# Kernel optimization log

Measured on AMD Instinct MI355X. Metric: run time of the kernel, lower is better.

The kernel has to match this reference:

```python
import jax, jax.numpy as jnp
import numpy as np

KER = 8

def _gelu(x):
    return jax.nn.gelu(x, approximate=False)

def _conv3x3(x, w, b):
    y = jax.lax.conv_general_dilated(x, w, (1, 1), 'SAME',
                                     dimension_numbers=('NCHW', 'OIHW', 'NCHW'))
    return y + b[None, :, None, None]

def _unfold(x):
    # F.unfold(kernel=8, stride=8): [B,C,H,W] -> [B, C*64, L], C-major then kh,kw
    B, C, H, W = x.shape
    Hb, Wb = H // KER, W // KER
    p = x.reshape(B, C, Hb, KER, Wb, KER).transpose(0, 1, 3, 5, 2, 4)
    return p.reshape(B, C * KER * KER, Hb * Wb)

def _fold(cols, H, W):
    # inverse of _unfold (non-overlapping patches)
    B, CK, L = cols.shape
    C = CK // (KER * KER)
    Hb, Wb = H // KER, W // KER
    p = cols.reshape(B, C, KER, KER, Hb, Wb).transpose(0, 1, 4, 2, 5, 3)
    return p.reshape(B, C, H, W)

def _bn(x, g, b, eps=1e-5):
    # train-mode BatchNorm1d on [B, C, L]: stats over (B, L) per channel
    m = x.mean(axis=(0, 2), keepdims=True)
    v = x.var(axis=(0, 2), keepdims=True)
    return (x - m) * jax.lax.rsqrt(v + eps) * g[None, :, None] + b[None, :, None]


def setup_inputs() -> dict:
    key = jax.random.key(0)
    ks = jax.random.split(key, 10)
    ind, d, hid = 64, 1024, 256
    f = lambda k, s: jax.random.normal(k, s, dtype=jnp.float32) * 0.02
    return {
        'feat': jax.random.normal(ks[0], (4, ind, 256, 256), dtype=jnp.float32),
        'w_enc': f(ks[1], (ind, ind, 3, 3)), 'b_enc': jnp.zeros((ind,), jnp.float32),
        'w_k': f(ks[2], (ind, ind, 3, 3)), 'b_k': jnp.zeros((ind,), jnp.float32),
        'w_v': f(ks[3], (ind, ind, 3, 3)), 'b_v': jnp.zeros((ind,), jnp.float32),
        'fcq_w': f(ks[4], (d, ind * KER * KER)), 'fcq_b': jnp.zeros((d,), jnp.float32),
        'fck_w': f(ks[5], (d, ind * KER * KER)), 'fck_b': jnp.zeros((d,), jnp.float32),
        'bnq_g': jnp.ones((d,), jnp.float32), 'bnq_b': jnp.zeros((d,), jnp.float32),
        'bnk_g': jnp.ones((d,), jnp.float32), 'bnk_b': jnp.zeros((d,), jnp.float32),
        'ff1_w': f(ks[6], (hid, ind)), 'ff1_b': jnp.zeros((hid,), jnp.float32),
        'ff2_w': f(ks[7], (ind, hid)), 'ff2_b': jnp.zeros((ind,), jnp.float32),
    }


def reference(feat, w_enc, b_enc, w_k, b_k, w_v, b_v,
              fcq_w, fcq_b, fck_w, fck_b, bnq_g, bnq_b, bnk_g, bnk_b,
              ff1_w, ff1_b, ff2_w, ff2_b):
    B, C, H, W = feat.shape
    fk = _gelu(_conv3x3(feat, w_k, b_k))
    fv = _gelu(_conv3x3(feat, w_v, b_v))
    refer = _gelu(_conv3x3(feat, w_enc, b_enc))
    q_un = _unfold(refer).transpose(0, 2, 1)   # [B, L, C*64]
    k_un = _unfold(fk).transpose(0, 2, 1)
    v_un = _unfold(fv).transpose(0, 2, 1)
    q = jnp.einsum('blc,dc->bld', q_un, fcq_w) + fcq_b
    q = _bn(q.transpose(0, 2, 1), bnq_g, bnq_b).transpose(0, 2, 1)  # [B, L, 1024]
    k = jnp.einsum('blc,dc->bld', k_un, fck_w) + fck_b
    k = _bn(k.transpose(0, 2, 1), bnk_g, bnk_b).transpose(0, 2, 1)
    scores = jnp.einsum('bld,bmd->blm', q, k) / jnp.sqrt(jnp.float32(q.shape[2]))
    attn = jax.nn.softmax(scores, axis=2)
    out = jnp.einsum('blm,bmc->blc', attn, v_un).transpose(0, 2, 1)  # [B, C*64, L]
    out = _fold(out, H, W)
    h = _gelu(jnp.einsum('bchw,oc->bohw', out, ff1_w) + ff1_b[None, :, None, None])
    h = _gelu(jnp.einsum('bchw,oc->bohw', h, ff2_w) + ff2_b[None, :, None, None])
    return h + feat
```

## Files before the change

kernel.cpp:

```cpp
#include <hip/hip_runtime.h>

typedef unsigned short u16;
typedef float f4 __attribute__((ext_vector_type(4)));
typedef float f32x4 __attribute__((ext_vector_type(4)));
typedef short bf16x8 __attribute__((ext_vector_type(8)));
typedef u16 u16x8 __attribute__((ext_vector_type(8)));
typedef u16 u16x4 __attribute__((ext_vector_type(4)));

__device__ __forceinline__ u16 f2bf(float f){
  unsigned u = __float_as_uint(f);
  u = (u + 0x7FFFu + ((u>>16)&1u)) >> 16;
  return (u16)u;
}
__device__ __forceinline__ float bf2f(u16 u){
  return __uint_as_float(((unsigned)u)<<16);
}
__device__ __forceinline__ float gelu_f(float x){
  float y = 1.5957691216057308f*(x + 0.044715f*x*x*x);
  y = fminf(y, 30.0f);
  float t = __expf(y);
  float r = __builtin_amdgcn_rcpf(t + 1.0f);
  return 0.5f*x*(1.0f + (t - 1.0f)*r);
}

typedef __attribute__((address_space(1))) const unsigned int as1_cuint;
typedef __attribute__((address_space(3))) unsigned int as3_uint;
__device__ __forceinline__ void gload_lds16(const void* g, void* l){
  __builtin_amdgcn_global_load_lds((as1_cuint*)g, (as3_uint*)l, 16, 0, 0);
}

__global__ __launch_bounds__(256) void to_nhwc(
    const float* __restrict__ F, u16* __restrict__ O)
{
  __shared__ float tile[64][65];
  const int t = threadIdx.x, b = blockIdx.y;
  const long px0 = (long)blockIdx.x*64;
  const float* Fb = F + (long)b*64*65536;
  #pragma unroll
  for (int i = 0; i < 4; ++i){
    const int ch = (t>>4) + i*16;
    const int pxo = (t&15)*4;
    f4 v = *(const f4*)&Fb[(long)ch*65536 + px0 + pxo];
    tile[ch][pxo]=v[0]; tile[ch][pxo+1]=v[1]; tile[ch][pxo+2]=v[2]; tile[ch][pxo+3]=v[3];
  }
  __syncthreads();
  const int px = t & 63, ch0 = (t>>6)*16;
  u16x8 o0, o1;
  #pragma unroll
  for (int j = 0; j < 8; ++j){ o0[j]=f2bf(tile[ch0+j][px]); o1[j]=f2bf(tile[ch0+8+j][px]); }
  u16* Ob = O + ((long)b*65536 + px0 + px)*64 + ch0;
  *(u16x8*)Ob = o0; *(u16x8*)(Ob+8) = o1;
}

__global__ __launch_bounds__(256) void wt_prep(
    const float* __restrict__ we, const float* __restrict__ wk,
    const float* __restrict__ wv, u16* __restrict__ Wt2)
{
  const int i = blockIdx.x*256 + threadIdx.x;
  const int cio = i & 31;
  const int t1 = i >> 5;
  const int n  = t1 % 192;
  const int t2 = t1 / 192;
  const int kc = t2 & 1, p = t2 >> 1;
  const int dy = p/3, dx = p - dy*3;
  const int ci = kc*32 + cio;
  const float* W = (n < 64) ? we : (n < 128) ? wk : wv;
  const int co = n & 63;
  Wt2[i] = f2bf(W[((co*64 + ci)*3 + dy)*3 + dx]);
}

__global__ __launch_bounds__(512,2) void conv_mfma(
    const u16* __restrict__ X, const u16* __restrict__ Wt2,
    const float* __restrict__ be, const float* __restrict__ bk, const float* __restrict__ bv,
    u16* __restrict__ Aq, u16* __restrict__ Ak, u16* __restrict__ Vl)
{
  __shared__ __align__(16) u16 smem[24576];
  const int t = threadIdx.x, lane = t & 63, wvi = t >> 6;
  const int bx = blockIdx.x, by = blockIdx.y, b = blockIdx.z;
  const int x0 = bx*16, y0 = by*8;
  const u16* Xb = X + (long)b*4194304;

  #pragma unroll
  for (int j = 0; j < 3; ++j){
    const int id = t + j*512;
    if (id < 1440){
      const int row = id / 144, rem = id - row*144, col = rem >> 3, ck = rem & 7;
      const int y = y0 - 1 + row, x = x0 - 1 + col;
      int4 v = {0,0,0,0};
      if ((unsigned)y < 256u && (unsigned)x < 256u)
        v = *(const int4*)(Xb + ((long)y*256 + x)*64 + ck*8);
      *(int4*)&smem[((row*18 + col)*8 + (ck ^ (col&7)))*8] = v;
    }
  }
  __syncthreads();

  const int wm4 = (wvi>>2)*4;
  const int wn  = (wvi&3)*48;
  const int fr = lane & 15, fo = lane >> 4;
  f32x4 acc[4][3] = {};

  #pragma unroll
  for (int dy = 0; dy < 3; ++dy)
  #pragma unroll
  for (int dx = 0; dx < 3; ++dx){
    const int p = dy*3 + dx;
    #pragma unroll
    for (int kc = 0; kc < 2; ++kc){
      bf16x8 af[4], bfv[3];
      const u16* wp = Wt2 + ((long)(p*2 + kc)*192 + wn + fr)*32 + fo*8;
      #pragma unroll
      for (int ni = 0; ni < 3; ++ni)
        bfv[ni] = *(const bf16x8*)(wp + ni*16*32);
      #pragma unroll
      for (int mi = 0; mi < 4; ++mi){
        const int row = wm4 + mi + dy;
        const int col = fr + dx;
        af[mi] = *(const bf16x8*)&smem[((row*18 + col)*8 + ((kc*4+fo) ^ (col&7)))*8];
      }
      #pragma unroll
      for (int mi = 0; mi < 4; ++mi)
        #pragma unroll
        for (int ni = 0; ni < 3; ++ni)
          acc[mi][ni] = __builtin_amdgcn_mfma_f32_16x16x32_bf16(af[mi], bfv[ni], acc[mi][ni], 0, 0, 0);
    }
  }
  __syncthreads();

  const int c0 = fo*4;
  const int lloc = c0 >> 3, kw0 = c0 & 7;
  #pragma unroll
  for (int ni = 0; ni < 3; ++ni){
    const int n = wn + ni*16 + fr;
    const int mat = n >> 6, co = n & 63;
    const float bias = (mat==0) ? be[co] : (mat==1) ? bk[co] : bv[co];
    #pragma unroll
    for (int mi = 0; mi < 4; ++mi){
      const int r = wm4 + mi;
      u16x4 o;
      #pragma unroll
      for (int rg = 0; rg < 4; ++rg) o[rg] = f2bf(gelu_f(acc[mi][ni][rg] + bias));
      const int e = ((mat*2 + lloc)*64 + co)*64 + ((r*8 + kw0) ^ ((co&7)<<3));
      *(u16x4*)&smem[e] = o;
    }
  }
  __syncthreads();

  const int l_lo = by*32 + bx*2;
  const int co_r = t >> 3, sw = (t&7) ^ (co_r&7);
  const int eoff = co_r*64 + sw*8;
  #pragma unroll
  for (int i = 0; i < 6; ++i){
    const int mat = i >> 1, ll = i & 1;
    u16x8 v = *(const u16x8*)&smem[(mat*2 + ll)*4096 + eoff];
    u16* dst = (mat==0 ? Aq : mat==1 ? Ak : Vl)
             + ((long)b*1024 + l_lo + ll)*4096 + t*8;
    *(u16x8*)dst = v;
  }
}

__global__ __launch_bounds__(256) void v_tr(
    const u16* __restrict__ S, u16* __restrict__ D)
{
  __shared__ u16 tl[64][72];
  const int t = threadIdx.x, b = blockIdx.z;
  const int ck0 = blockIdx.x*64, l0 = blockIdx.y*64;
  const u16* Sb = S + (long)b*4194304;
  u16* Db = D + (long)b*4194304;
  #pragma unroll
  for (int j = 0; j < 2; ++j){
    const int li = (t>>3) + j*32, cko = (t&7)*8;
    *(u16x8*)&tl[li][cko] = *(const u16x8*)(Sb + (long)(l0+li)*4096 + ck0 + cko);
  }
  __syncthreads();
  #pragma unroll
  for (int j = 0; j < 2; ++j){
    const int cki = (t>>3) + j*32, lo = (t&7)*8;
    u16x8 v;
    #pragma unroll
    for (int e = 0; e < 8; ++e) v[e] = tl[lo+e][cki];
    *(u16x8*)(Db + (long)(ck0+cki)*1024 + l0 + lo) = v;
  }
}

template<int EPI>
__global__ __launch_bounds__(256,2) void gemm_bt(
    const u16* __restrict__ A, long sA,
    const u16* __restrict__ B, long sB, const int zshB,
    void* __restrict__ Cv, long sC,
    const int M, const int N, const int K,
    float* __restrict__ bnstats)
{
  const int bI = blockIdx.z;
  const u16* Ab = A + (long)bI*sA;
  const u16* Bb = B + (long)(bI>>zshB)*sB;
  const int m0 = blockIdx.x*128, n0 = blockIdx.y*128;
  __shared__ __align__(16) u16 As[128*32];
  __shared__ __align__(16) u16 Bs[128*32];
  const int t = threadIdx.x, lane = t & 63, wv = t >> 6;
  const int wm = (wv>>1)*64, wn = (wv&1)*64;
  const int fr = lane & 15, fo = lane >> 4;
  f32x4 acc[4][4] = {};
  const int c0 = wv*128 + lane, c1 = c0 + 64;
  const u16* Ag0 = Ab + (long)(m0 + (c0>>2))*K + (c0&3)*8;
  const u16* Ag1 = Ab + (long)(m0 + (c1>>2))*K + (c1&3)*8;
  const u16* Bg0 = Bb + (long)(n0 + (c0>>2))*K + (c0&3)*8;
  const u16* Bg1 = Bb + (long)(n0 + (c1>>2))*K + (c1&3)*8;
  u16* lA0 = &As[wv*1024];
  u16* lA1 = &As[wv*1024 + 512];
  u16* lB0 = &Bs[wv*1024];
  u16* lB1 = &Bs[wv*1024 + 512];
  for (int k0 = 0; k0 < K; k0 += 32){
    __syncthreads();
    gload_lds16(Ag0 + k0, lA0);
    gload_lds16(Ag1 + k0, lA1);
    gload_lds16(Bg0 + k0, lB0);
    gload_lds16(Bg1 + k0, lB1);
    __syncthreads();
    bf16x8 af[4], bfv[4];
    #pragma unroll
    for (int i = 0; i < 4; ++i){
      af[i]  = *(const bf16x8*)&As[(wm + i*16 + fr)*32 + fo*8];
      bfv[i] = *(const bf16x8*)&Bs[(wn + i*16 + fr)*32 + fo*8];
    }
    #pragma unroll
    for (int mi = 0; mi < 4; ++mi)
      #pragma unroll
      for (int ni = 0; ni < 4; ++ni)
        acc[mi][ni] = __builtin_amdgcn_mfma_f32_16x16x32_bf16(af[mi], bfv[ni], acc[mi][ni], 0, 0, 0);
  }
  if (EPI == 0){
    float* Cf = (float*)Cv + (long)bI*sC;
    #pragma unroll
    for (int mi = 0; mi < 4; ++mi)
      #pragma unroll
      for (int ni = 0; ni < 4; ++ni){
        const int col = n0 + wn + ni*16 + fr;
        #pragma unroll
        for (int r = 0; r < 4; ++r){
          const int row = m0 + wm + mi*16 + fo*4 + r;
          Cf[(long)row*N + col] = acc[mi][ni][r];
        }
      }
  } else if (EPI == 1) {
    u16* O = (u16*)Cv;
    #pragma unroll
    for (int mi = 0; mi < 4; ++mi)
      #pragma unroll
      for (int ni = 0; ni < 4; ++ni){
        const int col = n0 + wn + ni*16 + fr;
        const int c = col >> 6, khh = (col>>3)&7, kww = col&7;
        #pragma unroll
        for (int r = 0; r < 4; ++r){
          const int row = m0 + wm + mi*16 + fo*4 + r;
          const int hb = row >> 5, wbb = row & 31;
          O[(((long)bI*65536 + (hb*8+khh)*256 + wbb*8 + kww)<<6) + c] = f2bf(acc[mi][ni][r]);
        }
      }
  } else {
    u16* Cb = (u16*)Cv + (long)bI*sC;
    #pragma unroll
    for (int mi = 0; mi < 4; ++mi)
      #pragma unroll
      for (int ni = 0; ni < 4; ++ni){
        const int col = n0 + wn + ni*16 + fr;
        const int row0 = m0 + wm + mi*16 + fo*4;
        u16x4 o;
        #pragma unroll
        for (int r = 0; r < 4; ++r) o[r] = f2bf(acc[mi][ni][r]);
        *(u16x4*)&Cb[(long)col*M + row0] = o;
      }
    const int sel = bI >> 2;
    float* sums = bnstats + sel*2048;
    #pragma unroll
    for (int ni = 0; ni < 4; ++ni){
      float s = 0.f, q = 0.f;
      #pragma unroll
      for (int mi = 0; mi < 4; ++mi)
        #pragma unroll
        for (int r = 0; r < 4; ++r){
          const float v = acc[mi][ni][r];
          s += v; q += v*v;
        }
      s += __shfl_xor(s, 16); s += __shfl_xor(s, 32);
      q += __shfl_xor(q, 16); q += __shfl_xor(q, 32);
      if (fo == 0){
        const int col = n0 + wn + ni*16 + fr;
        atomicAdd(&sums[col], s);
        atomicAdd(&sums[1024 + col], q);
      }
    }
  }
}

__global__ __launch_bounds__(256,3) void ff1_mfma(
    const u16* __restrict__ X, const u16* __restrict__ W1b,
    const float* __restrict__ B1, u16* __restrict__ H1)
{
  const int t = threadIdx.x, lane = t & 63, wv = t >> 6;
  const long m0 = (long)blockIdx.x*128 + (wv>>1)*64;
  const int n0 = blockIdx.y*128 + (wv&1)*64;
  const int fr = lane & 15, fo = lane >> 4;
  f32x4 acc[4][4] = {};
  #pragma unroll
  for (int k0 = 0; k0 < 64; k0 += 32){
    bf16x8 af[4], bfv[4];
    #pragma unroll
    for (int i = 0; i < 4; ++i){
      af[i]  = *(const bf16x8*)(X   + (m0 + i*16 + fr)*64 + k0 + fo*8);
      bfv[i] = *(const bf16x8*)(W1b + (long)(n0 + i*16 + fr)*64 + k0 + fo*8);
    }
    #pragma unroll
    for (int mi = 0; mi < 4; ++mi)
      #pragma unroll
      for (int ni = 0; ni < 4; ++ni)
        acc[mi][ni] = __builtin_amdgcn_mfma_f32_16x16x32_bf16(af[mi], bfv[ni], acc[mi][ni], 0, 0, 0);
  }
  #pragma unroll
  for (int ni = 0; ni < 4; ++ni){
    const int col = n0 + ni*16 + fr;
    const float bc = B1[col];
    #pragma unroll
    for (int mi = 0; mi < 4; ++mi){
      const long row = m0 + mi*16 + fo*4;
      #pragma unroll
      for (int r = 0; r < 4; ++r)
        H1[(row + r)*256 + col] = f2bf(gelu_f(acc[mi][ni][r] + bc));
    }
  }
}

__global__ __launch_bounds__(256,3) void ff2_mfma(
    const u16* __restrict__ H1, const u16* __restrict__ W2b,
    const float* __restrict__ B2, const float* __restrict__ F,
    float* __restrict__ OUT)
{
  const int t = threadIdx.x, lane = t & 63, wv = t >> 6;
  const long m0 = (long)blockIdx.x*256 + wv*64;
  const int fr = lane & 15, fo = lane >> 4;
  f32x4 acc[4][4] = {};
  for (int k0 = 0; k0 < 256; k0 += 32){
    bf16x8 af[4], bfv[4];
    #pragma unroll
    for (int i = 0; i < 4; ++i){
      af[i]  = *(const bf16x8*)(H1  + (m0 + i*16 + fr)*256 + k0 + fo*8);
      bfv[i] = *(const bf16x8*)(W2b + (long)(i*16 + fr)*256 + k0 + fo*8);
    }
    #pragma unroll
    for (int mi = 0; mi < 4; ++mi)
      #pragma unroll
      for (int ni = 0; ni < 4; ++ni)
        acc[mi][ni] = __builtin_amdgcn_mfma_f32_16x16x32_bf16(af[mi], bfv[ni], acc[mi][ni], 0, 0, 0);
  }
  #pragma unroll
  for (int ni = 0; ni < 4; ++ni){
    const int c = ni*16 + fr;
    const float bc = B2[c];
    #pragma unroll
    for (int mi = 0; mi < 4; ++mi){
      const long p = m0 + mi*16 + fo*4;
      const int b = (int)(p >> 16), pp = (int)(p & 65535);
      const long idx = ((long)(b*64 + c))*65536 + pp;
      const f4 fres = *(const f4*)&F[idx];
      f4 o;
      #pragma unroll
      for (int r = 0; r < 4; ++r) o[r] = gelu_f(acc[mi][ni][r] + bc) + fres[r];
      *(f4*)&OUT[idx] = o;
    }
  }
}

__global__ __launch_bounds__(256) void cvt_w(
    const float* __restrict__ Wq, const float* __restrict__ Wk,
    u16* __restrict__ Oq, u16* __restrict__ Ok)
{
  const long i = ((long)blockIdx.x*256 + threadIdx.x)*4;
  const float* s = blockIdx.y ? Wk : Wq;
  u16* d = blockIdx.y ? Ok : Oq;
  f4 v = *(const f4*)&s[i];
  u16x4 o; o[0]=f2bf(v[0]); o[1]=f2bf(v[1]); o[2]=f2bf(v[2]); o[3]=f2bf(v[3]);
  *(u16x4*)&d[i] = o;
}

__global__ __launch_bounds__(256) void cvt_ffw(
    const float* __restrict__ W1, const float* __restrict__ W2,
    u16* __restrict__ O1, u16* __restrict__ O2)
{
  const long i = ((long)blockIdx.x*256 + threadIdx.x)*4;
  const float* s = blockIdx.y ? W2 : W1;
  u16* d = blockIdx.y ? O2 : O1;
  f4 v = *(const f4*)&s[i];
  u16x4 o; o[0]=f2bf(v[0]); o[1]=f2bf(v[1]); o[2]=f2bf(v[2]); o[3]=f2bf(v[3]);
  *(u16x4*)&d[i] = o;
}

__global__ void bn_fin2(float* __restrict__ stats,
                        const float* __restrict__ gq, const float* __restrict__ bq,
                        const float* __restrict__ gk, const float* __restrict__ bk)
{
  const int sel = blockIdx.y;
  const int d = blockIdx.x*256 + threadIdx.x;
  if (d >= 1024) return;
  const float* sum   = stats + sel*2048;
  const float* sumsq = sum + 1024;
  const float* g    = sel ? gk : gq;
  const float* beta = sel ? bk : bq;
  const float m  = sum[d]   * (1.f/4096.f);
  const float vv = sumsq[d] * (1.f/4096.f) - m*m;
  const float sc = g[d] * rsqrtf(vv + 1e-5f);
  stats[4096 + sel*2048 + d]        = sc;
  stats[4096 + sel*2048 + 1024 + d] = beta[d] - m*sc;
}

__global__ __launch_bounds__(256) void bn_apply_t(
    const u16* __restrict__ QT, const float* __restrict__ stats,
    u16* __restrict__ Y)
{
  __shared__ u16 tl[64][72];
  const int t = threadIdx.x, zi = blockIdx.z;
  const int d0 = blockIdx.x*64, l0 = blockIdx.y*64;
  const int sel = zi >> 2;
  const u16* S = QT + (long)zi*1048576;
  u16* D = Y + (long)zi*1048576;
  const float* scp = stats + 4096 + sel*2048;
  const float* shp = scp + 1024;
  #pragma unroll
  for (int j = 0; j < 2; ++j){
    const int di = (t>>3) + j*32, lo = (t&7)*8;
    const int d = d0 + di;
    const float sc = scp[d], sh = shp[d];
    u16x8 v = *(const u16x8*)(S + (long)d*1024 + l0 + lo);
    u16x8 o;
    #pragma unroll
    for (int e = 0; e < 8; ++e) o[e] = f2bf(bf2f(v[e])*sc + sh);
    *(u16x8*)&tl[di][lo] = o;
  }
  __syncthreads();
  #pragma unroll
  for (int j = 0; j < 2; ++j){
    const int li = (t>>3) + j*32, dof = (t&7)*8;
    u16x8 v;
    #pragma unroll
    for (int e = 0; e < 8; ++e) v[e] = tl[dof+e][li];
    *(u16x8*)(D + (long)(l0+li)*1024 + d0 + dof) = v;
  }
}

__global__ __launch_bounds__(256) void softmax_k(
    const float* __restrict__ S, u16* __restrict__ P)
{
  const long row = blockIdx.x;
  const float* p = S + row*1024;
  const int t = threadIdx.x;
  f4 v = *(const f4*)&p[t*4];
  v *= 0.03125f;
  float mx = fmaxf(fmaxf(v[0],v[1]), fmaxf(v[2],v[3]));
  #pragma unroll
  for (int o = 1; o < 64; o <<= 1) mx = fmaxf(mx, __shfl_xor(mx, o));
  __shared__ float red[4], red2[4];
  if ((t & 63) == 0) red[t>>6] = mx;
  __syncthreads();
  mx = fmaxf(fmaxf(red[0],red[1]), fmaxf(red[2],red[3]));
  f4 e;
  e[0]=__expf(v[0]-mx); e[1]=__expf(v[1]-mx); e[2]=__expf(v[2]-mx); e[3]=__expf(v[3]-mx);
  float sm = e[0]+e[1]+e[2]+e[3];
  #pragma unroll
  for (int o = 1; o < 64; o <<= 1) sm += __shfl_xor(sm, o);
  if ((t & 63) == 0) red2[t>>6] = sm;
  __syncthreads();
  sm = red2[0]+red2[1]+red2[2]+red2[3];
  const float inv = 1.0f/sm;
  u16x4 o4; o4[0]=f2bf(e[0]*inv); o4[1]=f2bf(e[1]*inv); o4[2]=f2bf(e[2]*inv); o4[3]=f2bf(e[3]*inv);
  *(u16x4*)&P[row*1024 + t*4] = o4;
}

extern "C" void kernel_launch(void* const* d_in, const int* in_sizes, int n_in,
                              void* d_out, int out_size, void* d_ws, size_t ws_size,
                              hipStream_t stream)
{
  const float* feat  = (const float*)d_in[0];
  const float* w_enc = (const float*)d_in[1];
  const float* b_enc = (const float*)d_in[2];
  const float* w_k   = (const float*)d_in[3];
  const float* b_k   = (const float*)d_in[4];
  const float* w_v   = (const float*)d_in[5];
  const float* b_v   = (const float*)d_in[6];
  const float* fcq_w = (const float*)d_in[7];
  const float* fck_w = (const float*)d_in[9];
  const float* bnq_g = (const float*)d_in[11];
  const float* bnq_b = (const float*)d_in[12];
  const float* bnk_g = (const float*)d_in[13];
  const float* bnk_b = (const float*)d_in[14];
  const float* ff1w  = (const float*)d_in[15];
  const float* ff1b  = (const float*)d_in[16];
  const float* ff2w  = (const float*)d_in[17];
  const float* ff2b  = (const float*)d_in[18];

  char* ws = (char*)d_ws;
  u16*   Aq      = (u16*)  (ws);
  u16*   Ak      = (u16*)  (ws + (32ull<<20));
  u16*   Vc      = (u16*)  (ws + (64ull<<20));
  u16*   Wq      = (u16*)  (ws + (96ull<<20));
  u16*   Wk      = (u16*)  (ws + (104ull<<20));
  u16*   q_bf    = (u16*)  (ws + (112ull<<20));
  u16*   k_bf    = (u16*)  (ws + (120ull<<20));
  u16*   qk_rawT = (u16*)  (ws + (128ull<<20));
  float* scores  = (float*)(ws + (160ull<<20));
  u16*   attn    = (u16*)  (ws + (176ull<<20));
  u16*   out_nhwc= (u16*)  (ws + (184ull<<20));
  u16*   NX      = (u16*)  (ws + (128ull<<20));
  u16*   Vl      = (u16*)  (ws + (160ull<<20));
  u16*   Wt2     = (u16*)  (ws + (216ull<<20));
  float* stats   = (float*)(ws + (217ull<<20));
  u16*   W1b     = (u16*)  (ws + (218ull<<20));
  u16*   W2b     = (u16*)  (ws + (218ull<<20) + 65536);
  u16*   h1      = (u16*)  (ws);

  hipMemsetAsync(stats, 0, 4096*sizeof(float), stream);

  to_nhwc<<<dim3(1024,4), 256, 0, stream>>>(feat, NX);
  wt_prep<<<dim3(432), 256, 0, stream>>>(w_enc, w_k, w_v, Wt2);
  conv_mfma<<<dim3(16,32,4), 512, 0, stream>>>(NX, Wt2, b_enc, b_k, b_v, Aq, Ak, Vl);
  v_tr<<<dim3(64,16,4), 256, 0, stream>>>(Vl, Vc);
  cvt_w<<<dim3(4096,2), 256, 0, stream>>>(fcq_w, fck_w, Wq, Wk);
  cvt_ffw<<<dim3(16,2), 256, 0, stream>>>(ff1w, ff2w, W1b, W2b);

  gemm_bt<2><<<dim3(8,8,8),  256, 0, stream>>>(Aq, 4194304, Wq, 4194304, 2,
                                               qk_rawT, 1048576, 1024, 1024, 4096, stats);

  bn_fin2<<<dim3(4,2), 256, 0, stream>>>(stats, bnq_g, bnq_b, bnk_g, bnk_b);
  bn_apply_t<<<dim3(16,16,8), 256, 0, stream>>>(qk_rawT, stats, q_bf);

  gemm_bt<0><<<dim3(8,8,4),  256, 0, stream>>>(q_bf, 1048576, k_bf, 1048576, 0,
                                               scores, 1048576, 1024, 1024, 1024, nullptr);
  softmax_k<<<dim3(4096), 256, 0, stream>>>(scores, attn);

  gemm_bt<1><<<dim3(8,32,4), 256, 0, stream>>>(attn, 1048576, Vc, 4194304, 0,
                                               out_nhwc, 0, 1024, 4096, 1024, nullptr);

  ff1_mfma<<<dim3(2048,2), 256, 0, stream>>>(out_nhwc, W1b, ff1b, h1);
  ff2_mfma<<<dim3(1024), 256, 0, stream>>>(h1, W2b, ff2b, feat, (float*)d_out);
}
```

Measured before the change: 535.2 us.

## Double-buffer LDS tiles in gemm_bt and raise launch-bounds occupancy to three

The GEMM main loop now uses two LDS buffers. It prefetches the next K-slice with async global-to-LDS loads while MFMAs run on the current slice, which drops one of the two barriers per iteration. Launch bounds go from 2 to 3 blocks per CU to allow more resident waves. This doubles LDS use to 32KB per block and tightens the register budget, which could cause spills or leave the occupancy gain unused.

```diff
diff --git a/kernel.cpp b/kernel.cpp
--- a/kernel.cpp
+++ b/kernel.cpp
@@ -183,7 +183,7 @@
 }
 
 template<int EPI>
-__global__ __launch_bounds__(256,2) void gemm_bt(
+__global__ __launch_bounds__(256,3) void gemm_bt(
     const u16* __restrict__ A, long sA,
     const u16* __restrict__ B, long sB, const int zshB,
     void* __restrict__ Cv, long sC,
@@ -194,8 +194,8 @@
   const u16* Ab = A + (long)bI*sA;
   const u16* Bb = B + (long)(bI>>zshB)*sB;
   const int m0 = blockIdx.x*128, n0 = blockIdx.y*128;
-  __shared__ __align__(16) u16 As[128*32];
-  __shared__ __align__(16) u16 Bs[128*32];
+  __shared__ __align__(16) u16 As[8192];
+  __shared__ __align__(16) u16 Bs[8192];
   const int t = threadIdx.x, lane = t & 63, wv = t >> 6;
   const int wm = (wv>>1)*64, wn = (wv&1)*64;
   const int fr = lane & 15, fo = lane >> 4;
@@ -205,28 +205,36 @@
   const u16* Ag1 = Ab + (long)(m0 + (c1>>2))*K + (c1&3)*8;
   const u16* Bg0 = Bb + (long)(n0 + (c0>>2))*K + (c0&3)*8;
   const u16* Bg1 = Bb + (long)(n0 + (c1>>2))*K + (c1&3)*8;
-  u16* lA0 = &As[wv*1024];
-  u16* lA1 = &As[wv*1024 + 512];
-  u16* lB0 = &Bs[wv*1024];
-  u16* lB1 = &Bs[wv*1024 + 512];
-  for (int k0 = 0; k0 < K; k0 += 32){
+  const int lo0 = wv*1024;
+  gload_lds16(Ag0, &As[lo0]);
+  gload_lds16(Ag1, &As[lo0 + 512]);
+  gload_lds16(Bg0, &Bs[lo0]);
+  gload_lds16(Bg1, &Bs[lo0 + 512]);
+  const int nk = K >> 5;
+  int cur = 0;
+  for (int ki = 0; ki < nk; ++ki){
     __syncthreads();
-    gload_lds16(Ag0 + k0, lA0);
-    gload_lds16(Ag1 + k0, lA1);
-    gload_lds16(Bg0 + k0, lB0);
-    gload_lds16(Bg1 + k0, lB1);
-    __syncthreads();
+    if (ki + 1 < nk){
+      const int k0 = (ki + 1) << 5;
+      const int so = ((cur^1) << 12) + lo0;
+      gload_lds16(Ag0 + k0, &As[so]);
+      gload_lds16(Ag1 + k0, &As[so + 512]);
+      gload_lds16(Bg0 + k0, &Bs[so]);
+      gload_lds16(Bg1 + k0, &Bs[so + 512]);
+    }
+    const int ro = cur << 12;
     bf16x8 af[4], bfv[4];
     #pragma unroll
     for (int i = 0; i < 4; ++i){
-      af[i]  = *(const bf16x8*)&As[(wm + i*16 + fr)*32 + fo*8];
-      bfv[i] = *(const bf16x8*)&Bs[(wn + i*16 + fr)*32 + fo*8];
+      af[i]  = *(const bf16x8*)&As[ro + (wm + i*16 + fr)*32 + fo*8];
+      bfv[i] = *(const bf16x8*)&Bs[ro + (wn + i*16 + fr)*32 + fo*8];
     }
     #pragma unroll
     for (int mi = 0; mi < 4; ++mi)
       #pragma unroll
       for (int ni = 0; ni < 4; ++ni)
         acc[mi][ni] = __builtin_amdgcn_mfma_f32_16x16x32_bf16(af[mi], bfv[ni], acc[mi][ni], 0, 0, 0);
+    cur ^= 1;
   }
   if (EPI == 0){
     float* Cf = (float*)Cv + (long)bI*sC;
```

After: 537.8 us. About the same (+0.5%).
